# Kernel tuning notes

Measured on AMD Instinct MI355X. Metric: run time of the kernel, lower is better.

Reference implementation:

```python
import jax, jax.numpy as jnp
import numpy as np

MAXDISP = 48  # module stores maxdisp + 1 = 49 disparity planes


def setup_inputs() -> dict:
    key = jax.random.key(0)
    k1, k2 = jax.random.split(key)
    B, C, H, W = 4, 320, 128, 240
    x = jax.random.normal(k1, (B, C, H, W), dtype=jnp.float32)
    y = jax.random.normal(k2, (B, C, H, W), dtype=jnp.float32)
    return {"x": x, "y": y}


def _cost_volume(x, y, maxdisp):
    # x, y: [B, C, H, W]. For each disparity i: channel-sum correlation of
    # x shifted right against y, left-padded with zeros to width W.
    b, c, h, w = x.shape
    D = maxdisp + 1
    costs = [(x * y).sum(axis=1)]  # [B, H, W], disparity 0
    for i in range(1, D):
        corr = (x[:, :, :, i:] * y[:, :, :, : w - i]).sum(axis=1)  # [B, H, W-i]
        costs.append(jnp.pad(corr, ((0, 0), (0, 0), (i, 0))))
    # torch cats [1,B,H,W] slices along dim 1 (disp-major) then unsqueeze(0)
    cost = jnp.stack(costs, axis=0)            # [D, B, H, W]
    return cost.reshape(1, 1, D * b, h, w)     # [1, 1, D*B, H, W]


def reference(x, y):
    return _cost_volume(x, y, MAXDISP)
```

## Files before the change

### kernel.cpp

```cpp
#include <hip/hip_runtime.h>
#include <stdint.h>
#include <stddef.h>

#define NB 4
#define NC 320
#define NH 128
#define NW 240
#define ND 49
#define HW (NH * NW)
#define CC 32
#define NCHUNK (NC / CC)
#define XMAX 128
#define YMAX 160
#define BUFSZ ((XMAX + YMAX) * CC)

typedef float f32x4 __attribute__((ext_vector_type(4)));
typedef short s16x8 __attribute__((ext_vector_type(8)));

__device__ __forceinline__ uint32_t bf16r(float f) {
  uint32_t u = __builtin_bit_cast(uint32_t, f);
  return (u + 0x7FFFu + ((u >> 16) & 1u)) >> 16;
}
__device__ __forceinline__ int swz(int w) { return (w ^ (w >> 2)) & 3; }

template <int HALF>
__device__ __forceinline__ void cv_body(const float* __restrict__ xrow,
                                        const float* __restrict__ yrow,
                                        float* __restrict__ orow,
                                        short* lds, const int tid) {
  constexpr int WT0   = HALF ? 8   : 0;
  constexpr int XW0   = HALF ? 128 : 0;
  constexpr int XCOLS = HALF ? 112 : 128;
  constexpr int YW0   = HALF ? 80  : 0;
  constexpr int YCOLS = HALF ? 160 : 128;
  constexpr int NW4X  = XCOLS / 4;
  constexpr int NW4Y  = YCOLS / 4;

  const int wave = tid >> 6;
  const int l = tid & 63;
  const int m = l & 15;
  const int q = l >> 4;

  int u_arr, u_w4, u_c8;
  if (tid < XCOLS) { u_arr = 0; u_w4 = tid % NW4X; u_c8 = tid / NW4X; }
  else             { const int v = tid - XCOLS; u_arr = 1; u_w4 = v % NW4Y; u_c8 = v / NW4Y; }
  const float* u_src = (u_arr ? yrow : xrow) + (u_arr ? YW0 : XW0) + u_w4 * 4;
  const int u_lds = u_arr ? XMAX * CC : 0;

  const bool has_e = (HALF == 1) && ((tid & 15) == 0);
  const int e_w4 = 24 + (tid >> 4);
  const float* e_src = yrow + YW0 + e_w4 * 4;

  f32x4 acc[2][4] = {};

  auto stage = [&](int buf, int chunk) {
    {
      const float* p = u_src + (size_t)(chunk * CC + u_c8 * 8) * HW;
      f32x4 val[8];
#pragma unroll
      for (int j = 0; j < 8; ++j) val[j] = *(const f32x4*)(p + (size_t)j * HW);
      short* base = lds + buf * BUFSZ + u_lds;
#pragma unroll
      for (int idx = 0; idx < 4; ++idx) {
        const int ww = (idx + u_w4) & 3;
        const int w = u_w4 * 4 + ww;
        s16x8 s;
#pragma unroll
        for (int j = 0; j < 8; ++j) s[j] = (short)bf16r(val[j][ww]);
        *(s16x8*)&base[w * CC + ((u_c8 ^ swz(w)) * 8)] = s;
      }
    }
    if (has_e) {
      const float* p2 = e_src + (size_t)(chunk * CC + 24) * HW;
      f32x4 val2[8];
#pragma unroll
      for (int j = 0; j < 8; ++j) val2[j] = *(const f32x4*)(p2 + (size_t)j * HW);
      short* base = lds + buf * BUFSZ + XMAX * CC;
#pragma unroll
      for (int idx = 0; idx < 4; ++idx) {
        const int ww = (idx + e_w4) & 3;
        const int w = e_w4 * 4 + ww;
        s16x8 s;
#pragma unroll
        for (int j = 0; j < 8; ++j) s[j] = (short)bf16r(val2[j][ww]);
        *(s16x8*)&base[w * CC + ((3 ^ swz(w)) * 8)] = s;
      }
    }
  };

  auto compute = [&](int buf) {
    const short* bx = lds + buf * BUFSZ;
    const short* by = lds + buf * BUFSZ + XMAX * CC;
#pragma unroll
    for (int i = 0; i < 2; ++i) {
      const int wt = WT0 + wave * 2 + i;
      if (HALF == 1 && wt > 14) continue;
      const int war = wt * 16 + m - XW0;
      const s16x8 a = *(const s16x8*)&bx[war * CC + ((q ^ swz(war)) * 8)];
#pragma unroll
      for (int ss = 0; ss < 4; ++ss) {
        const int st = wt - 3 + ss;
        if (HALF == 1 || st >= 0) {
          const int wbr = st * 16 + m - YW0;
          const s16x8 bb = *(const s16x8*)&by[wbr * CC + ((q ^ swz(wbr)) * 8)];
          acc[i][ss] = __builtin_amdgcn_mfma_f32_16x16x32_bf16(a, bb, acc[i][ss], 0, 0, 0);
        }
      }
    }
  };

  stage(0, 0);
  __syncthreads();
  for (int k = 0; k < NCHUNK; ++k) {
    if (k + 1 < NCHUNK) stage((k + 1) & 1, k + 1);
    compute(k & 1);
    __syncthreads();
  }

#pragma unroll
  for (int i = 0; i < 2; ++i) {
    const int wt = WT0 + wave * 2 + i;
    if (HALF == 1 && wt > 14) continue;
#pragma unroll
    for (int ss = 0; ss < 4; ++ss) {
      const int st = wt - 3 + ss;
      const int wj = st * 16 + m;
#pragma unroll
      for (int r = 0; r < 4; ++r) {
        const int wi = wt * 16 + q * 4 + r;
        const int d = wi - wj;
        if (d >= 0 && d < ND) {
          const float v = (st >= 0) ? acc[i][ss][r] : 0.0f;
          orow[(size_t)d * (NB * HW) + wi] = v;
        }
      }
    }
  }
}

__global__ __launch_bounds__(256)
__attribute__((amdgpu_waves_per_eu(4, 4)))
void cv_kernel(const float* __restrict__ X,
               const float* __restrict__ Y,
               float* __restrict__ O) {
  __shared__ short lds[2 * BUFSZ];
  const int tid = threadIdx.x;
  const int bid = blockIdx.x;
  const int logical = (bid & 7) * 128 + (bid >> 3);
  const int row = logical >> 1;
  const int half = logical & 1;
  const int b = row >> 7, h = row & 127;
  const float* xrow = X + (size_t)b * NC * HW + (size_t)h * NW;
  const float* yrow = Y + (size_t)b * NC * HW + (size_t)h * NW;
  float* orow = O + ((size_t)b * NH + h) * NW;
  if (half == 0) cv_body<0>(xrow, yrow, orow, lds, tid);
  else           cv_body<1>(xrow, yrow, orow, lds, tid);
}

extern "C" void kernel_launch(void* const* d_in, const int* in_sizes, int n_in,
                              void* d_out, int out_size, void* d_ws, size_t ws_size,
                              hipStream_t stream) {
  const float* x = (const float*)d_in[0];
  const float* y = (const float*)d_in[1];
  float* out = (float*)d_out;
  cv_kernel<<<dim3(1024), dim3(256), 0, stream>>>(x, y, out);
}
```

Baseline: 83.14 us.

## Split each row into three segments and software-pipeline global loads two chunks ahead

Each image row is now split into three 80-column segments instead of two halves, which raises the grid from 1024 to 1536 blocks and shrinks the per-block LDS footprint. The staging is restructured so that each wave loads its own 8-channel slice into registers two chunks ahead, converts it to bf16, and writes it to LDS after compute. This hides global-load latency behind the MFMA work. In exchange, more y columns are re-read from global memory because neighbouring segments overlap, and only some lanes per wave take part in loading.

```diff
diff --git a/kernel.cpp b/kernel.cpp
--- a/kernel.cpp
+++ b/kernel.cpp
@@ -10,9 +10,9 @@
 #define HW (NH * NW)
 #define CC 32
 #define NCHUNK (NC / CC)
-#define XMAX 128
-#define YMAX 160
-#define BUFSZ ((XMAX + YMAX) * CC)
+#define XMAXC 80
+#define YMAXC 128
+#define BUFSZ ((XMAXC + YMAXC) * CC)
 
 typedef float f32x4 __attribute__((ext_vector_type(4)));
 typedef short s16x8 __attribute__((ext_vector_type(8)));
@@ -23,84 +23,72 @@
 }
 __device__ __forceinline__ int swz(int w) { return (w ^ (w >> 2)) & 3; }
 
-template <int HALF>
+template <int SEG>
 __device__ __forceinline__ void cv_body(const float* __restrict__ xrow,
                                         const float* __restrict__ yrow,
                                         float* __restrict__ orow,
                                         short* lds, const int tid) {
-  constexpr int WT0   = HALF ? 8   : 0;
-  constexpr int XW0   = HALF ? 128 : 0;
-  constexpr int XCOLS = HALF ? 112 : 128;
-  constexpr int YW0   = HALF ? 80  : 0;
-  constexpr int YCOLS = HALF ? 160 : 128;
-  constexpr int NW4X  = XCOLS / 4;
+  constexpr int WT0   = SEG * 5;
+  constexpr int XW0   = SEG * 80;
+  constexpr int YW0   = (SEG == 0) ? 0 : SEG * 80 - 48;
+  constexpr int YCOLS = (SEG == 0) ? 80 : 128;
+  constexpr int NW4X  = XMAXC / 4;
   constexpr int NW4Y  = YCOLS / 4;
+  constexpr int UPW   = NW4X + NW4Y;
 
   const int wave = tid >> 6;
   const int l = tid & 63;
   const int m = l & 15;
   const int q = l >> 4;
 
-  int u_arr, u_w4, u_c8;
-  if (tid < XCOLS) { u_arr = 0; u_w4 = tid % NW4X; u_c8 = tid / NW4X; }
-  else             { const int v = tid - XCOLS; u_arr = 1; u_w4 = v % NW4Y; u_c8 = v / NW4Y; }
-  const float* u_src = (u_arr ? yrow : xrow) + (u_arr ? YW0 : XW0) + u_w4 * 4;
-  const int u_lds = u_arr ? XMAX * CC : 0;
-
-  const bool has_e = (HALF == 1) && ((tid & 15) == 0);
-  const int e_w4 = 24 + (tid >> 4);
-  const float* e_src = yrow + YW0 + e_w4 * 4;
+  const bool act = l < UPW;
+  const bool isX = l < NW4X;
+  const int u_w4 = isX ? l : (l - NW4X);
+  const float* u_src = (isX ? xrow + XW0 : yrow + YW0) + u_w4 * 4;
+  const int u_lds_off = isX ? 0 : XMAXC * CC;
 
   f32x4 acc[2][4] = {};
+  f32x4 L[8];
+  s16x8 P[4];
 
-  auto stage = [&](int buf, int chunk) {
-    {
-      const float* p = u_src + (size_t)(chunk * CC + u_c8 * 8) * HW;
-      f32x4 val[8];
+  auto load_chunk = [&](int chunk) {
+    const float* p = u_src + (size_t)(chunk * CC + wave * 8) * HW;
 #pragma unroll
-      for (int j = 0; j < 8; ++j) val[j] = *(const f32x4*)(p + (size_t)j * HW);
-      short* base = lds + buf * BUFSZ + u_lds;
+    for (int j = 0; j < 8; ++j) L[j] = *(const f32x4*)(p + (size_t)j * HW);
+  };
+  auto convert = [&]() {
 #pragma unroll
-      for (int idx = 0; idx < 4; ++idx) {
-        const int ww = (idx + u_w4) & 3;
-        const int w = u_w4 * 4 + ww;
-        s16x8 s;
+    for (int ww = 0; ww < 4; ++ww) {
+      s16x8 s;
 #pragma unroll
-        for (int j = 0; j < 8; ++j) s[j] = (short)bf16r(val[j][ww]);
-        *(s16x8*)&base[w * CC + ((u_c8 ^ swz(w)) * 8)] = s;
-      }
+      for (int j = 0; j < 8; ++j) s[j] = (short)bf16r(L[j][ww]);
+      P[ww] = s;
     }
-    if (has_e) {
-      const float* p2 = e_src + (size_t)(chunk * CC + 24) * HW;
-      f32x4 val2[8];
+  };
+  auto write_P = [&](int buf) {
+    short* base = lds + buf * BUFSZ + u_lds_off;
 #pragma unroll
-      for (int j = 0; j < 8; ++j) val2[j] = *(const f32x4*)(p2 + (size_t)j * HW);
-      short* base = lds + buf * BUFSZ + XMAX * CC;
-#pragma unroll
-      for (int idx = 0; idx < 4; ++idx) {
-        const int ww = (idx + e_w4) & 3;
-        const int w = e_w4 * 4 + ww;
-        s16x8 s;
-#pragma unroll
-        for (int j = 0; j < 8; ++j) s[j] = (short)bf16r(val2[j][ww]);
-        *(s16x8*)&base[w * CC + ((3 ^ swz(w)) * 8)] = s;
-      }
+    for (int idx = 0; idx < 4; ++idx) {
+      const int ww = (idx + u_w4) & 3;
+      const int w = u_w4 * 4 + ww;
+      *(s16x8*)&base[w * CC + (((wave ^ swz(w)) & 3) * 8)] = P[ww];
     }
   };
 
   auto compute = [&](int buf) {
     const short* bx = lds + buf * BUFSZ;
-    const short* by = lds + buf * BUFSZ + XMAX * CC;
+    const short* by = lds + buf * BUFSZ + XMAXC * CC;
 #pragma unroll
     for (int i = 0; i < 2; ++i) {
-      const int wt = WT0 + wave * 2 + i;
-      if (HALF == 1 && wt > 14) continue;
-      const int war = wt * 16 + m - XW0;
+      const int wtl = wave + i * 4;
+      if (wtl > 4) continue;
+      const int wt = WT0 + wtl;
+      const int war = wtl * 16 + m;
       const s16x8 a = *(const s16x8*)&bx[war * CC + ((q ^ swz(war)) * 8)];
 #pragma unroll
       for (int ss = 0; ss < 4; ++ss) {
         const int st = wt - 3 + ss;
-        if (HALF == 1 || st >= 0) {
+        if (SEG > 0 || st >= 0) {
           const int wbr = st * 16 + m - YW0;
           const s16x8 bb = *(const s16x8*)&by[wbr * CC + ((q ^ swz(wbr)) * 8)];
           acc[i][ss] = __builtin_amdgcn_mfma_f32_16x16x32_bf16(a, bb, acc[i][ss], 0, 0, 0);
@@ -109,18 +97,24 @@
     }
   };
 
-  stage(0, 0);
+  if (act) { load_chunk(0); convert(); load_chunk(1); write_P(0); }
   __syncthreads();
+
   for (int k = 0; k < NCHUNK; ++k) {
-    if (k + 1 < NCHUNK) stage((k + 1) & 1, k + 1);
+    if (act && k + 1 < NCHUNK) {
+      convert();
+      if (k + 2 < NCHUNK) load_chunk(k + 2);
+    }
     compute(k & 1);
+    if (act && k + 1 < NCHUNK) write_P((k + 1) & 1);
     __syncthreads();
   }
 
 #pragma unroll
   for (int i = 0; i < 2; ++i) {
-    const int wt = WT0 + wave * 2 + i;
-    if (HALF == 1 && wt > 14) continue;
+    const int wtl = wave + i * 4;
+    if (wtl > 4) continue;
+    const int wt = WT0 + wtl;
 #pragma unroll
     for (int ss = 0; ss < 4; ++ss) {
       const int st = wt - 3 + ss;
@@ -146,15 +140,16 @@
   __shared__ short lds[2 * BUFSZ];
   const int tid = threadIdx.x;
   const int bid = blockIdx.x;
-  const int logical = (bid & 7) * 128 + (bid >> 3);
-  const int row = logical >> 1;
-  const int half = logical & 1;
+  const int logical = (bid & 7) * 192 + (bid >> 3);
+  const int row = logical / 3;
+  const int seg = logical % 3;
   const int b = row >> 7, h = row & 127;
   const float* xrow = X + (size_t)b * NC * HW + (size_t)h * NW;
   const float* yrow = Y + (size_t)b * NC * HW + (size_t)h * NW;
   float* orow = O + ((size_t)b * NH + h) * NW;
-  if (half == 0) cv_body<0>(xrow, yrow, orow, lds, tid);
-  else           cv_body<1>(xrow, yrow, orow, lds, tid);
+  if (seg == 0)      cv_body<0>(xrow, yrow, orow, lds, tid);
+  else if (seg == 1) cv_body<1>(xrow, yrow, orow, lds, tid);
+  else               cv_body<2>(xrow, yrow, orow, lds, tid);
 }
 
 extern "C" void kernel_launch(void* const* d_in, const int* in_sizes, int n_in,
@@ -163,5 +158,5 @@
   const float* x = (const float*)d_in[0];
   const float* y = (const float*)d_in[1];
   float* out = (float*)d_out;
-  cv_kernel<<<dim3(1024), dim3(256), 0, stream>>>(x, y, out);
+  cv_kernel<<<dim3(1536), dim3(256), 0, stream>>>(x, y, out);
 }
```

Result: slower. 243.6 us (+193.0%).
